# Kernel tuning notes

Hardware: AMD Instinct MI355X
Metric: run time of the kernel (lower is better)

The kernel has to match this reference:

```python
import jax, jax.numpy as jnp
import numpy as np

NH = 1024
VS = 50257
CUT0 = 1675          # round(VS/30)
CUT1 = 3 * CUT0      # 5025
N_CLUSTERS = 2
HEAD_SIZE = CUT0 + N_CLUSTERS          # 1677
D0, D1 = NH // 4, NH // 16             # 256, 64
SZ0, SZ1 = CUT1 - CUT0, VS - CUT1      # 3350, 45232


def setup_inputs() -> dict:
    key = jax.random.key(0)
    ks = jax.random.split(key, 8)
    s = 0.02
    return {
        "x": jax.random.normal(ks[0], (8, 512, NH), dtype=jnp.float32),
        "y": jax.random.randint(ks[1], (8, 512), 0, VS, dtype=jnp.int64),
        "head_w": jax.random.normal(ks[2], (HEAD_SIZE, NH), dtype=jnp.float32) * s,
        "head_b": jnp.zeros((HEAD_SIZE,), dtype=jnp.float32),
        "proj0": jax.random.normal(ks[3], (D0, NH), dtype=jnp.float32) * s,
        "w0": jax.random.normal(ks[4], (SZ0, D0), dtype=jnp.float32) * s,
        "proj1": jax.random.normal(ks[5], (D1, NH), dtype=jnp.float32) * s,
        "w1": jax.random.normal(ks[6], (SZ1, D1), dtype=jnp.float32) * s,
    }


def reference(x, y, head_w, head_b, proj0, w0, proj1, w1):
    # Flatten as in the torch forward: x -> [N, nh], y -> [N]
    xf = x.reshape(-1, x.shape[-1])            # [N, NH]
    yf = y.reshape(-1)                         # [N]

    # Head: shortlist tokens + 2 cluster logits
    head_logits = jnp.einsum('nh,vh->nv', xf, head_w) + head_b   # [N, 1677]
    head_lp = jax.nn.log_softmax(head_logits, axis=-1)

    # Default: target in head shortlist
    in_head = yf < CUT0
    idx_head = jnp.where(in_head, yf, 0)
    out = jnp.take_along_axis(head_lp, idx_head[:, None], axis=1)[:, 0]

    # Tail clusters: dense per-cluster small GEMMs + log-softmax, masked select
    for i, (low, high, proj, w) in enumerate(
            [(CUT0, CUT1, proj0, w0), (CUT1, VS, proj1, w1)]):
        size = high - low
        h = jnp.einsum('nh,dh->nd', xf, proj)          # [N, d_i]
        lp = jax.nn.log_softmax(jnp.einsum('nd,vd->nv', h, w), axis=-1)  # [N, size]
        rel = jnp.clip(yf - low, 0, size - 1)
        cl = head_lp[:, CUT0 + i] + jnp.take_along_axis(lp, rel[:, None], axis=1)[:, 0]
        mask = (yf >= low) & (yf < high)
        out = jnp.where(mask, cl, out)

    loss = -jnp.mean(out)
    return out, loss
```

## Files before the change

### kernel.cpp

```cpp
#include <hip/hip_runtime.h>
#include <stdint.h>

#define NROWS 4096
#define NHID 1024
#define CC0 1675
#define CC1 5025
#define HEADSZ 1677
#define PD0 256
#define PD1 64
#define TSZ0 3350
#define TSZ1 45232
#define HPN (HEADSZ + PD0 + PD1)
#define TPC1 6
#define L2E 1.4426950408889634f
#define LN2 0.6931471805599453f

#define NB_HD 448
#define NB_PJ 96
#define NB_CW 512
#define NB_MID (NB_HD + NB_PJ + NB_CW)

#define NB_C0 864
#define NB_C1 1888
#define NB_TG 1024
#define NB_TAIL (NB_C0 + NB_C1 + NB_TG)

typedef __attribute__((ext_vector_type(8))) __bf16 bf16x8;
typedef __attribute__((ext_vector_type(4))) float f32x4;

__device__ __forceinline__ unsigned short f2bf(float f) {
  union { float f; uint32_t u; } v; v.f = f;
  return (unsigned short)((v.u + 0x7FFFu + ((v.u >> 16) & 1u)) >> 16);
}
__device__ __forceinline__ float bfl(uint32_t u) {
  union { uint32_t u; float f; } v; v.u = u << 16; return v.f;
}
__device__ __forceinline__ float bfh(uint32_t u) {
  union { uint32_t u; float f; } v; v.u = u & 0xFFFF0000u; return v.f;
}
__device__ __forceinline__ float bf1(unsigned short u) {
  union { uint32_t u; float f; } v; v.u = ((uint32_t)u) << 16; return v.f;
}
#define EXP2(x) __builtin_amdgcn_exp2f(x)

#define CV1 1048576
#define CV2 1477888
#define CV3 1543424
#define CV4 1559808
#define CV5 1774208
#define CV6 2497920
#define CVW0 (CV5 - CV4)
#define CVW  (CV6 - CV4)

__global__ void conv_part(const float* __restrict__ x, const float* __restrict__ hw,
                          const float* __restrict__ p0, const float* __restrict__ p1,
                          unsigned short* __restrict__ dst) {
  int stride = gridDim.x * blockDim.x;
  for (int i = blockIdx.x * blockDim.x + threadIdx.x; i < CV4; i += stride) {
    const float* src; int off; float sc;
    if (i < CV1)      { src = x;  off = i;       sc = 1.f; }
    else if (i < CV2) { src = hw; off = i - CV1; sc = L2E; }
    else if (i < CV3) { src = p0; off = i - CV2; sc = 1.f; }
    else              { src = p1; off = i - CV3; sc = 1.f; }
    float4 v = reinterpret_cast<const float4*>(src)[off];
    ushort4 o;
    o.x = f2bf(v.x * sc); o.y = f2bf(v.y * sc);
    o.z = f2bf(v.z * sc); o.w = f2bf(v.w * sc);
    reinterpret_cast<ushort4*>(dst)[i] = o;
  }
}

#define GLOAD(g, l) __builtin_amdgcn_global_load_lds( \
    (const __attribute__((address_space(1))) uint32_t*)(const void*)(g), \
    (__attribute__((address_space(3))) uint32_t*)(void*)(l), 16, 0, 0)

#define SWZB(L) ((L) ^ ((((L) >> 7) & 7) << 4))

__device__ __forceinline__
void gemm_core(const unsigned short* __restrict__ A, int lda,
               const unsigned short* __restrict__ B, int ldb,
               int N, int K, int tile0, int tile1, int brow,
               const float* __restrict__ bias,
               float* __restrict__ sum_out,
               unsigned short* __restrict__ Cout, int ldc, int coutStart,
               unsigned short* AsB, unsigned short* BsB) {
  const int tid = threadIdx.x;
  const int lane = tid & 63;
  const int wid = tid >> 6;
  const int wrow = (wid >> 1) * 64;
  const int wcol = (wid & 1) * 64;
  const int lr = lane & 15, lg = lane >> 4;
  const int nsteps = (tile1 - tile0) * (K >> 5);
  const int rowBase = brow + wrow;

  float sacc[4][4];
#pragma unroll
  for (int m = 0; m < 4; ++m)
#pragma unroll
    for (int r = 0; r < 4; ++r) sacc[m][r] = 0.f;

  auto stage = [&](int b, int tt, int kk) {
#pragma unroll
    for (int c = 0; c < 2; ++c) {
      int g = wid * 128 + c * 64 + lane;
      int L = g * 16;
      int S = SWZB(L);
      int row = S >> 6, ko = (S >> 4) & 3;
      GLOAD(A + (size_t)(brow + row) * lda + kk + ko * 8, (char*)AsB + b * 8192 + L);
      int bsrc = tt * 128 + row; bsrc = bsrc < N ? bsrc : N - 1;
      GLOAD(B + (size_t)bsrc * ldb + kk + ko * 8, (char*)BsB + b * 8192 + L);
    }
  };

  f32x4 acc[4][4];
#pragma unroll
  for (int m = 0; m < 4; ++m)
#pragma unroll
    for (int n = 0; n < 4; ++n) acc[m][n] = (f32x4){0.f, 0.f, 0.f, 0.f};

  int tp = tile0, kp = 0;
  auto adv = [&](int& t, int& k) { k += 32; if (k == K) { k = 0; ++t; } };
  stage(0, tp, kp); adv(tp, kp);
  if (nsteps > 1) { stage(1, tp, kp); adv(tp, kp); }

  int tile = tile0, k0 = 0;
  for (int s = 0; s < nsteps; ++s) {
    if (s + 1 < nsteps) asm volatile("s_waitcnt vmcnt(4)" ::: "memory");
    else                asm volatile("s_waitcnt vmcnt(0)" ::: "memory");
    __builtin_amdgcn_s_barrier();
    if (s + 2 < nsteps) { stage((s + 2) % 3, tp, kp); adv(tp, kp); }

    const int cur = s % 3;
    int k0n = k0 + 32, tn = tile;
    if (k0n == K) { k0n = 0; tn = tile + 1; }

    bf16x8 af[4], bfv[4];
#pragma unroll
    for (int m = 0; m < 4; ++m)
      af[m] = *(const bf16x8*)((const char*)AsB + cur * 8192 +
                               SWZB((wrow + m * 16 + lr) * 64 + lg * 16));
#pragma unroll
    for (int n = 0; n < 4; ++n)
      bfv[n] = *(const bf16x8*)((const char*)BsB + cur * 8192 +
                                SWZB((wcol + n * 16 + lr) * 64 + lg * 16));
#pragma unroll
    for (int m = 0; m < 4; ++m)
#pragma unroll
      for (int n = 0; n < 4; ++n)
        acc[m][n] = __builtin_amdgcn_mfma_f32_16x16x32_bf16(af[m], bfv[n], acc[m][n], 0, 0, 0);

    if (tn != tile) {
      const int cb = tile * 128 + wcol;
#pragma unroll
      for (int m = 0; m < 4; ++m)
#pragma unroll
        for (int n = 0; n < 4; ++n) {
#pragma unroll
          for (int r = 0; r < 4; ++r) {
            int col = cb + n * 16 + lr;
            if (col < N) {
              float v = acc[m][n][r];
              if (Cout && col >= coutStart) {
                int row = rowBase + m * 16 + lg * 4 + r;
                Cout[(size_t)row * ldc + (col - coutStart)] = f2bf(v);
              } else {
                if (bias) v = fmaf(bias[col], L2E, v);
                sacc[m][r] += EXP2(v);
              }
            }
          }
          acc[m][n] = (f32x4){0.f, 0.f, 0.f, 0.f};
        }
    }
    tile = tn; k0 = k0n;
  }

#pragma unroll
  for (int m = 0; m < 4; ++m)
#pragma unroll
    for (int r = 0; r < 4; ++r) {
      float s = sacc[m][r];
      s += __shfl_xor(s, 1); s += __shfl_xor(s, 2);
      s += __shfl_xor(s, 4); s += __shfl_xor(s, 8);
      if (lr == 0) atomicAdd(&sum_out[rowBase + m * 16 + lg * 4 + r], s);
    }
}

__global__ __launch_bounds__(256, 3)
void fused_mid(const unsigned short* __restrict__ xb,
               const unsigned short* __restrict__ hpb,
               const float* __restrict__ head_b,
               float* __restrict__ hs,
               unsigned short* __restrict__ hb,
               float* __restrict__ dm,
               const float* __restrict__ w0f, const float* __restrict__ w1f,
               unsigned short* __restrict__ dstAll) {
  __shared__ __align__(16) unsigned short lds[6 * 4096];
  const int bid = blockIdx.x;

  if (bid < NB_HD) {
    const int xcd = bid & 7;
    const int local = bid >> 3;
    const int rowBlk = xcd * 4 + local / 14;
    const int colChunk = local % 14;
    gemm_core(xb, NHID, hpb, NHID, HEADSZ, NHID, colChunk, colChunk + 1,
              rowBlk * 128, head_b, hs, nullptr, 0, 0, lds, lds + 3 * 4096);
    return;
  }

  if (bid < NB_HD + NB_PJ) {
    const int b1 = bid - NB_HD;
    const int cpx = NB_PJ >> 3;
    const int sid = (b1 & 7) * cpx + (b1 >> 3);
    const int rowBlk = sid & 31;
    const int colChunk = sid >> 5;
    gemm_core(xb, NHID, hpb + (size_t)HEADSZ * NHID, NHID, PD0 + PD1, NHID,
              colChunk, colChunk + 1, rowBlk * 128,
              nullptr, dm, hb, PD0 + PD1, 0, lds, lds + 3 * 4096);
    return;
  }

  {
    const int b2 = bid - NB_HD - NB_PJ;
    const int stride = NB_CW * 256;
    for (int i = b2 * 256 + (int)threadIdx.x; i < CVW; i += stride) {
      const float* src; int off;
      if (i < CVW0) { src = w0f; off = i; }
      else          { src = w1f; off = i - CVW0; }
      float4 v = reinterpret_cast<const float4*>(src)[off];
      ushort4 o;
      o.x = f2bf(v.x * L2E); o.y = f2bf(v.y * L2E);
      o.z = f2bf(v.z * L2E); o.w = f2bf(v.w * L2E);
      reinterpret_cast<ushort4*>(dstAll)[CV4 + i] = o;
    }
  }
}

__global__ __launch_bounds__(256, 3)
void fused_tail(const unsigned short* __restrict__ hb,
                const unsigned short* __restrict__ w0b,
                const unsigned short* __restrict__ w1b,
                const unsigned short* __restrict__ xb,
                const unsigned short* __restrict__ hwb,
                const float* __restrict__ head_b,
                const int* __restrict__ y,
                float* __restrict__ s0, float* __restrict__ s1,
                float* __restrict__ ht, float* __restrict__ tc) {
  __shared__ __align__(16) unsigned short lds[6 * 4096];
  const int bid = blockIdx.x;

  if (bid < NB_C0) {
    const int cpx = NB_C0 >> 3;
    const int sid = (bid & 7) * cpx + (bid >> 3);
    const int rowBlk = sid & 31;
    const int colChunk = sid >> 5;
    gemm_core(hb, PD0 + PD1, w0b, PD0, TSZ0, PD0, colChunk, colChunk + 1,
              rowBlk * 128, nullptr, s0, nullptr, 0, 0, lds, lds + 3 * 4096);
    return;
  }

  if (bid < NB_C0 + NB_C1) {
    const int b1 = bid - NB_C0;
    const int tid = threadIdx.x;
    const int lane = tid & 63;
    const int wid = tid >> 6;
    const int lr = lane & 15, lg = lane >> 4;
    const int cpx = NB_C1 >> 3;
    const int sid = (b1 & 7) * cpx + (b1 >> 3);
    const int rowBlk = sid & 31;
    const int colChunk = sid >> 5;
    const int rowBase = rowBlk * 128 + (wid >> 1) * 64;
    const int wcol = (wid & 1) * 64;
    const int tile0 = colChunk * TPC1;

    int colOff[4], srcOff[4];
#pragma unroll
    for (int c = 0; c < 4; ++c) {
      int L = (c * 256 + tid) * 16;
      int S = L ^ (((L >> 7) & 7) << 4);
      colOff[c] = S >> 7;
      srcOff[c] = (S & 127) >> 1;
    }
    auto stage = [&](int b, int t) {
#pragma unroll
      for (int c = 0; c < 4; ++c) {
        int gc = t * 128 + colOff[c];
        gc = gc < TSZ1 ? gc : TSZ1 - 1;
        GLOAD(w1b + (size_t)gc * PD1 + srcOff[c],
              (char*)lds + b * 16384 + (c * 256 + tid) * 16);
      }
    };

    bf16x8 af[4][2];
#pragma unroll
    for (int m = 0; m < 4; ++m) {
      const unsigned short* p = hb + PD0 +
          (size_t)(rowBase + m * 16 + lr) * (PD0 + PD1) + lg * 8;
      af[m][0] = *(const bf16x8*)p;
      af[m][1] = *(const bf16x8*)(p + 32);
    }

    float sacc[4][4];
#pragma unroll
    for (int m = 0; m < 4; ++m)
#pragma unroll
      for (int r = 0; r < 4; ++r) sacc[m][r] = 0.f;

    stage(0, tile0);
    stage(1, tile0 + 1);

#pragma unroll 1
    for (int s = 0; s < TPC1; ++s) {
      if (s + 1 < TPC1) asm volatile("s_waitcnt vmcnt(4)" ::: "memory");
      else              asm volatile("s_waitcnt vmcnt(0)" ::: "memory");
      __builtin_amdgcn_s_barrier();
      if (s + 2 < TPC1) stage((s + 2) % 3, tile0 + s + 2);

      const int cur = s % 3;
      const int cb = (tile0 + s) * 128 + wcol;
      const int full = (cb + 63 < TSZ1);

#pragma unroll
      for (int nh = 0; nh < 2; ++nh) {
        bf16x8 bf[2][2];
#pragma unroll
        for (int nn = 0; nn < 2; ++nn) {
          int ccol = wcol + (nh * 2 + nn) * 16 + lr;
#pragma unroll
          for (int kh = 0; kh < 2; ++kh) {
            int L = ccol * 128 + kh * 64 + lg * 16;
            bf[nn][kh] = *(const bf16x8*)((const char*)lds + cur * 16384 +
                                          (L ^ ((ccol & 7) << 4)));
          }
        }
        f32x4 acc[4][2];
#pragma unroll
        for (int m = 0; m < 4; ++m)
#pragma unroll
          for (int nn = 0; nn < 2; ++nn) {
            f32x4 a = (f32x4){0.f, 0.f, 0.f, 0.f};
            a = __builtin_amdgcn_mfma_f32_16x16x32_bf16(af[m][0], bf[nn][0], a, 0, 0, 0);
            a = __builtin_amdgcn_mfma_f32_16x16x32_bf16(af[m][1], bf[nn][1], a, 0, 0, 0);
            acc[m][nn] = a;
          }
        if (full) {
#pragma unroll
          for (int m = 0; m < 4; ++m)
#pragma unroll
            for (int r = 0; r < 4; ++r)
              sacc[m][r] += EXP2(acc[m][0][r]) + EXP2(acc[m][1][r]);
        } else {
#pragma unroll
          for (int m = 0; m < 4; ++m)
#pragma unroll
            for (int r = 0; r < 4; ++r) {
              float t = 0.f;
#pragma unroll
              for (int nn = 0; nn < 2; ++nn)
                if (cb + (nh * 2 + nn) * 16 + lr < TSZ1) t += EXP2(acc[m][nn][r]);
              sacc[m][r] += t;
            }
        }
      }
    }

#pragma unroll
    for (int m = 0; m < 4; ++m)
#pragma unroll
      for (int r = 0; r < 4; ++r) {
        float s = sacc[m][r];
        s += __shfl_xor(s, 1); s += __shfl_xor(s, 2);
        s += __shfl_xor(s, 4); s += __shfl_xor(s, 8);
        if (lr == 0) atomicAdd(&s1[rowBase + m * 16 + lg * 4 + r], s);
      }
    return;
  }

  {
    const int b2 = bid - NB_C0 - NB_C1;
    int row = b2 * 4 + (threadIdx.x >> 6);
    int lane = threadIdx.x & 63;
    int yv = y[row];
    int th = yv < CC0 ? yv : (yv < CC1 ? CC0 : CC0 + 1);

    const unsigned short* xr = xb + (size_t)row * NHID + lane * 16;
    const unsigned short* wr = hwb + (size_t)th * NHID + lane * 16;
    uint4 xa = *(const uint4*)xr,       wa = *(const uint4*)wr;
    uint4 xc = *(const uint4*)(xr + 8), wc = *(const uint4*)(wr + 8);
    float s = 0.f;
    uint32_t xs[8] = {xa.x, xa.y, xa.z, xa.w, xc.x, xc.y, xc.z, xc.w};
    uint32_t ws[8] = {wa.x, wa.y, wa.z, wa.w, wc.x, wc.y, wc.z, wc.w};
#pragma unroll
    for (int j = 0; j < 8; ++j)
      s += bfl(xs[j]) * bfl(ws[j]) + bfh(xs[j]) * bfh(ws[j]);
#pragma unroll
    for (int d = 1; d < 64; d <<= 1) s += __shfl_xor(s, d);

    float cl = 0.f;
    if (yv >= CC0) {
      if (yv < CC1) {
        int rel = yv - CC0;
        const unsigned short* hr = hb + (size_t)row * (PD0 + PD1) + lane * 4;
        const unsigned short* w0r = w0b + (size_t)rel * PD0 + lane * 4;
        uint2 ha = *(const uint2*)hr, wa0 = *(const uint2*)w0r;
        cl = bfl(ha.x) * bfl(wa0.x) + bfh(ha.x) * bfh(wa0.x)
           + bfl(ha.y) * bfl(wa0.y) + bfh(ha.y) * bfh(wa0.y);
      } else {
        int rel = yv - CC1;
        cl = bf1(hb[(size_t)row * (PD0 + PD1) + PD0 + lane])
           * bf1(w1b[(size_t)rel * PD1 + lane]);
      }
#pragma unroll
      for (int d = 1; d < 64; d <<= 1) cl += __shfl_xor(cl, d);
    }
    if (lane == 0) { ht[row] = s * LN2 + head_b[th]; tc[row] = (yv < CC0) ? 0.f : cl; }
  }
}

__global__ void rowloss(const float* __restrict__ hs, const float* __restrict__ ht,
                        const float* __restrict__ s0, const float* __restrict__ s1,
                        const float* __restrict__ tc,
                        const int* __restrict__ y, float* __restrict__ out) {
  int n = blockIdx.x * 256 + threadIdx.x;
  int yv = y[n];
  float o = ht[n] - __builtin_amdgcn_logf(hs[n]) * LN2;
  if (yv >= CC0)
    o += tc[n] * LN2 - __builtin_amdgcn_logf(yv < CC1 ? s0[n] : s1[n]) * LN2;
  out[n] = o;
  float l = o;
#pragma unroll
  for (int d = 1; d < 64; d <<= 1) l += __shfl_xor(l, d);
  __shared__ float red[4];
  if ((threadIdx.x & 63) == 0) red[threadIdx.x >> 6] = l;
  __syncthreads();
  if (threadIdx.x == 0)
    atomicAdd(&out[NROWS], -(red[0] + red[1] + red[2] + red[3]) / (float)NROWS);
}

extern "C" void kernel_launch(void* const* d_in, const int* in_sizes, int n_in,
                              void* d_out, int out_size, void* d_ws, size_t ws_size,
                              hipStream_t stream) {
  const float* x      = (const float*)d_in[0];
  const int*   y      = (const int*)d_in[1];
  const float* head_w = (const float*)d_in[2];
  const float* head_b = (const float*)d_in[3];
  const float* proj0  = (const float*)d_in[4];
  const float* w0     = (const float*)d_in[5];
  const float* proj1  = (const float*)d_in[6];
  const float* w1     = (const float*)d_in[7];
  float* out = (float*)d_out;

  char* wp = (char*)d_ws;
  unsigned short* xb  = (unsigned short*)wp; wp += (size_t)NROWS * NHID * 2;
  unsigned short* hpb = (unsigned short*)wp; wp += (size_t)HPN * NHID * 2;
  unsigned short* w0b = (unsigned short*)wp; wp += (size_t)TSZ0 * PD0 * 2;
  unsigned short* w1b = (unsigned short*)wp; wp += (size_t)TSZ1 * PD1 * 2;
  unsigned short* hb  = (unsigned short*)wp; wp += (size_t)NROWS * (PD0 + PD1) * 2;
  float* hs = (float*)wp; wp += NROWS * 4;
  float* s0 = (float*)wp; wp += NROWS * 4;
  float* s1 = (float*)wp; wp += NROWS * 4;
  float* ht = (float*)wp; wp += NROWS * 4;
  float* tc = (float*)wp; wp += NROWS * 4;
  float* dm = (float*)wp; wp += NROWS * 4;

  hipMemsetAsync(hs, 0, 3 * NROWS * 4, stream);
  hipMemsetAsync(out + NROWS, 0, 4, stream);

  conv_part<<<dim3(1024), 256, 0, stream>>>(x, head_w, proj0, proj1, xb);

  fused_mid<<<dim3(NB_MID), 256, 0, stream>>>(
      xb, hpb, head_b, hs, hb, dm, w0, w1, xb);

  fused_tail<<<dim3(NB_TAIL), 256, 0, stream>>>(
      hb, w0b, w1b, xb, hpb, head_b, y, s0, s1, ht, tc);

  rowloss<<<dim3(NROWS / 256), 256, 0, stream>>>(hs, ht, s0, s1, tc, y, out);
}
```

Measured before the change: 104.9 us.

## Run tail kernel with 512-thread blocks and 8 waves per tile

The tail kernel now launches 512-thread blocks. Each 128x128 output tile is split across 8 waves, each owning 64 rows by 32 columns, instead of 4 waves owning 64 by 64. A new gemm_core512 variant handles the cluster-0 GEMM under the new layout, and the target-gather section now covers 8 rows per block with half as many blocks. The aim is more waves in flight and fewer accumulator registers per wave to hide latency, at the cost of more redundant A-fragment loads and barrier participants per tile.

```diff
diff --git a/kernel.cpp b/kernel.cpp
--- a/kernel.cpp
+++ b/kernel.cpp
@@ -22,7 +22,7 @@
 
 #define NB_C0 864
 #define NB_C1 1888
-#define NB_TG 1024
+#define NB_TG 512
 #define NB_TAIL (NB_C0 + NB_C1 + NB_TG)
 
 typedef __attribute__((ext_vector_type(8))) __bf16 bf16x8;
@@ -186,6 +186,92 @@
     }
 }
 
+__device__ __forceinline__
+void gemm_core512(const unsigned short* __restrict__ A, int lda,
+                  const unsigned short* __restrict__ B, int ldb,
+                  int N, int K, int tile0, int brow,
+                  float* __restrict__ sum_out,
+                  unsigned short* AsB, unsigned short* BsB) {
+  const int tid = threadIdx.x;
+  const int lane = tid & 63;
+  const int wid = tid >> 6;
+  const int wrow = (wid >> 2) * 64;
+  const int wcol = (wid & 3) * 32;
+  const int lr = lane & 15, lg = lane >> 4;
+  const int nsteps = K >> 5;
+  const int rowBase = brow + wrow;
+
+  float sacc[4][4];
+#pragma unroll
+  for (int m = 0; m < 4; ++m)
+#pragma unroll
+    for (int r = 0; r < 4; ++r) sacc[m][r] = 0.f;
+
+  const int L0 = tid * 16;
+  const int S0 = SWZB(L0);
+  const int arow = S0 >> 6, ako = ((S0 >> 4) & 3) * 8;
+
+  auto stage = [&](int b, int kk) {
+    GLOAD(A + (size_t)(brow + arow) * lda + kk + ako, (char*)AsB + b * 8192 + L0);
+    int bsrc = tile0 * 128 + arow; bsrc = bsrc < N ? bsrc : N - 1;
+    GLOAD(B + (size_t)bsrc * ldb + kk + ako, (char*)BsB + b * 8192 + L0);
+  };
+
+  f32x4 acc[4][2];
+#pragma unroll
+  for (int m = 0; m < 4; ++m)
+#pragma unroll
+    for (int n = 0; n < 2; ++n) acc[m][n] = (f32x4){0.f, 0.f, 0.f, 0.f};
+
+  stage(0, 0);
+  if (nsteps > 1) stage(1, 32);
+
+  for (int s = 0; s < nsteps; ++s) {
+    if (s + 1 < nsteps) asm volatile("s_waitcnt vmcnt(2)" ::: "memory");
+    else                asm volatile("s_waitcnt vmcnt(0)" ::: "memory");
+    __builtin_amdgcn_s_barrier();
+    if (s + 2 < nsteps) stage((s + 2) % 3, (s + 2) * 32);
+
+    const int cur = s % 3;
+    bf16x8 af[4], bfv[2];
+#pragma unroll
+    for (int m = 0; m < 4; ++m)
+      af[m] = *(const bf16x8*)((const char*)AsB + cur * 8192 +
+                               SWZB((wrow + m * 16 + lr) * 64 + lg * 16));
+#pragma unroll
+    for (int n = 0; n < 2; ++n)
+      bfv[n] = *(const bf16x8*)((const char*)BsB + cur * 8192 +
+                                SWZB((wcol + n * 16 + lr) * 64 + lg * 16));
+#pragma unroll
+    for (int m = 0; m < 4; ++m)
+#pragma unroll
+      for (int n = 0; n < 2; ++n)
+        acc[m][n] = __builtin_amdgcn_mfma_f32_16x16x32_bf16(af[m], bfv[n], acc[m][n], 0, 0, 0);
+  }
+
+  const int cb = tile0 * 128 + wcol;
+#pragma unroll
+  for (int m = 0; m < 4; ++m)
+#pragma unroll
+    for (int n = 0; n < 2; ++n) {
+      int col = cb + n * 16 + lr;
+      if (col < N) {
+#pragma unroll
+        for (int r = 0; r < 4; ++r) sacc[m][r] += EXP2(acc[m][n][r]);
+      }
+    }
+
+#pragma unroll
+  for (int m = 0; m < 4; ++m)
+#pragma unroll
+    for (int r = 0; r < 4; ++r) {
+      float s = sacc[m][r];
+      s += __shfl_xor(s, 1); s += __shfl_xor(s, 2);
+      s += __shfl_xor(s, 4); s += __shfl_xor(s, 8);
+      if (lr == 0) atomicAdd(&sum_out[rowBase + m * 16 + lg * 4 + r], s);
+    }
+}
+
 __global__ __launch_bounds__(256, 3)
 void fused_mid(const unsigned short* __restrict__ xb,
                const unsigned short* __restrict__ hpb,
@@ -236,7 +322,7 @@
   }
 }
 
-__global__ __launch_bounds__(256, 3)
+__global__ __launch_bounds__(512, 4)
 void fused_tail(const unsigned short* __restrict__ hb,
                 const unsigned short* __restrict__ w0b,
                 const unsigned short* __restrict__ w1b,
@@ -254,8 +340,8 @@
     const int sid = (bid & 7) * cpx + (bid >> 3);
     const int rowBlk = sid & 31;
     const int colChunk = sid >> 5;
-    gemm_core(hb, PD0 + PD1, w0b, PD0, TSZ0, PD0, colChunk, colChunk + 1,
-              rowBlk * 128, nullptr, s0, nullptr, 0, 0, lds, lds + 3 * 4096);
+    gemm_core512(hb, PD0 + PD1, w0b, PD0, TSZ0, PD0, colChunk,
+                 rowBlk * 128, s0, lds, lds + 3 * 4096);
     return;
   }
 
@@ -269,25 +355,25 @@
     const int sid = (b1 & 7) * cpx + (b1 >> 3);
     const int rowBlk = sid & 31;
     const int colChunk = sid >> 5;
-    const int rowBase = rowBlk * 128 + (wid >> 1) * 64;
-    const int wcol = (wid & 1) * 64;
+    const int rowBase = rowBlk * 128 + (wid >> 2) * 64;
+    const int wcol = (wid & 3) * 32;
     const int tile0 = colChunk * TPC1;
 
-    int colOff[4], srcOff[4];
-#pragma unroll
-    for (int c = 0; c < 4; ++c) {
-      int L = (c * 256 + tid) * 16;
+    int colOff[2], srcOff[2];
+#pragma unroll
+    for (int c = 0; c < 2; ++c) {
+      int L = (c * 512 + tid) * 16;
       int S = L ^ (((L >> 7) & 7) << 4);
       colOff[c] = S >> 7;
       srcOff[c] = (S & 127) >> 1;
     }
     auto stage = [&](int b, int t) {
 #pragma unroll
-      for (int c = 0; c < 4; ++c) {
+      for (int c = 0; c < 2; ++c) {
         int gc = t * 128 + colOff[c];
         gc = gc < TSZ1 ? gc : TSZ1 - 1;
         GLOAD(w1b + (size_t)gc * PD1 + srcOff[c],
-              (char*)lds + b * 16384 + (c * 256 + tid) * 16);
+              (char*)lds + b * 16384 + (c * 512 + tid) * 16);
       }
     };
 
@@ -311,56 +397,53 @@
 
 #pragma unroll 1
     for (int s = 0; s < TPC1; ++s) {
-      if (s + 1 < TPC1) asm volatile("s_waitcnt vmcnt(4)" ::: "memory");
+      if (s + 1 < TPC1) asm volatile("s_waitcnt vmcnt(2)" ::: "memory");
       else              asm volatile("s_waitcnt vmcnt(0)" ::: "memory");
       __builtin_amdgcn_s_barrier();
       if (s + 2 < TPC1) stage((s + 2) % 3, tile0 + s + 2);
 
       const int cur = s % 3;
       const int cb = (tile0 + s) * 128 + wcol;
-      const int full = (cb + 63 < TSZ1);
-
-#pragma unroll
-      for (int nh = 0; nh < 2; ++nh) {
-        bf16x8 bf[2][2];
+      const int full = (cb + 31 < TSZ1);
+
+      bf16x8 bf[2][2];
+#pragma unroll
+      for (int nn = 0; nn < 2; ++nn) {
+        int ccol = wcol + nn * 16 + lr;
+#pragma unroll
+        for (int kh = 0; kh < 2; ++kh) {
+          int L = ccol * 128 + kh * 64 + lg * 16;
+          bf[nn][kh] = *(const bf16x8*)((const char*)lds + cur * 16384 +
+                                        (L ^ ((ccol & 7) << 4)));
+        }
+      }
+      f32x4 acc[4][2];
+#pragma unroll
+      for (int m = 0; m < 4; ++m)
 #pragma unroll
         for (int nn = 0; nn < 2; ++nn) {
-          int ccol = wcol + (nh * 2 + nn) * 16 + lr;
-#pragma unroll
-          for (int kh = 0; kh < 2; ++kh) {
-            int L = ccol * 128 + kh * 64 + lg * 16;
-            bf[nn][kh] = *(const bf16x8*)((const char*)lds + cur * 16384 +
-                                          (L ^ ((ccol & 7) << 4)));
+          f32x4 a = (f32x4){0.f, 0.f, 0.f, 0.f};
+          a = __builtin_amdgcn_mfma_f32_16x16x32_bf16(af[m][0], bf[nn][0], a, 0, 0, 0);
+          a = __builtin_amdgcn_mfma_f32_16x16x32_bf16(af[m][1], bf[nn][1], a, 0, 0, 0);
+          acc[m][nn] = a;
+        }
+      if (full) {
+#pragma unroll
+        for (int m = 0; m < 4; ++m)
+#pragma unroll
+          for (int r = 0; r < 4; ++r)
+            sacc[m][r] += EXP2(acc[m][0][r]) + EXP2(acc[m][1][r]);
+      } else {
+#pragma unroll
+        for (int m = 0; m < 4; ++m)
+#pragma unroll
+          for (int r = 0; r < 4; ++r) {
+            float t = 0.f;
+#pragma unroll
+            for (int nn = 0; nn < 2; ++nn)
+              if (cb + nn * 16 + lr < TSZ1) t += EXP2(acc[m][nn][r]);
+            sacc[m][r] += t;
           }
-        }
-        f32x4 acc[4][2];
-#pragma unroll
-        for (int m = 0; m < 4; ++m)
-#pragma unroll
-          for (int nn = 0; nn < 2; ++nn) {
-            f32x4 a = (f32x4){0.f, 0.f, 0.f, 0.f};
-            a = __builtin_amdgcn_mfma_f32_16x16x32_bf16(af[m][0], bf[nn][0], a, 0, 0, 0);
-            a = __builtin_amdgcn_mfma_f32_16x16x32_bf16(af[m][1], bf[nn][1], a, 0, 0, 0);
-            acc[m][nn] = a;
-          }
-        if (full) {
-#pragma unroll
-          for (int m = 0; m < 4; ++m)
-#pragma unroll
-            for (int r = 0; r < 4; ++r)
-              sacc[m][r] += EXP2(acc[m][0][r]) + EXP2(acc[m][1][r]);
-        } else {
-#pragma unroll
-          for (int m = 0; m < 4; ++m)
-#pragma unroll
-            for (int r = 0; r < 4; ++r) {
-              float t = 0.f;
-#pragma unroll
-              for (int nn = 0; nn < 2; ++nn)
-                if (cb + (nh * 2 + nn) * 16 + lr < TSZ1) t += EXP2(acc[m][nn][r]);
-              sacc[m][r] += t;
-            }
-        }
       }
     }
 
@@ -378,7 +461,7 @@
 
   {
     const int b2 = bid - NB_C0 - NB_C1;
-    int row = b2 * 4 + (threadIdx.x >> 6);
+    int row = b2 * 8 + (threadIdx.x >> 6);
     int lane = threadIdx.x & 63;
     int yv = y[row];
     int th = yv < CC0 ? yv : (yv < CC1 ? CC0 : CC0 + 1);
@@ -471,7 +554,7 @@
   fused_mid<<<dim3(NB_MID), 256, 0, stream>>>(
       xb, hpb, head_b, hs, hb, dm, w0, w1, xb);
 
-  fused_tail<<<dim3(NB_TAIL), 256, 0, stream>>>(
+  fused_tail<<<dim3(NB_TAIL), 512, 0, stream>>>(
       hb, w0b, w1b, xb, hpb, head_b, y, s0, s1, ht, tc);
 
   rowloss<<<dim3(NROWS / 256), 256, 0, stream>>>(hs, ht, s0, s1, tc, y, out);
```

Result: slower. 119.4 us (+13.8%).

## Give each wave a private LDS slice in cluster-1 tail GEMM, drop block barriers

Applied to the files above, without the earlier changes.

Reworks the cluster-1 tail sum-of-exp GEMM so each wave stages its own 32-column slice of w1 into a private LDS region, so the per-tile block-wide barrier is no longer needed. Row blocks shrink to 64 rows and column chunks grow to 12 tiles, with a bounded tail chunk, giving 1920 blocks. The cluster-1 blocks now come first in the grid, ahead of the cluster-0 and target blocks. The aim is to cut barrier stalls and let the large tail work start early, at the cost of less cross-wave reuse of staged w1 data and more reloads of the h operand per column.

```diff
diff --git a/kernel.cpp b/kernel.cpp
--- a/kernel.cpp
+++ b/kernel.cpp
@@ -11,7 +11,8 @@
 #define TSZ0 3350
 #define TSZ1 45232
 #define HPN (HEADSZ + PD0 + PD1)
-#define TPC1 6
+#define NT1 354
+#define TPC1 12
 #define L2E 1.4426950408889634f
 #define LN2 0.6931471805599453f
 
@@ -20,10 +21,10 @@
 #define NB_CW 512
 #define NB_MID (NB_HD + NB_PJ + NB_CW)
 
+#define NB_C1 1920
 #define NB_C0 864
-#define NB_C1 1888
 #define NB_TG 1024
-#define NB_TAIL (NB_C0 + NB_C1 + NB_TG)
+#define NB_TAIL (NB_C1 + NB_C0 + NB_TG)
 
 typedef __attribute__((ext_vector_type(8))) __bf16 bf16x8;
 typedef __attribute__((ext_vector_type(4))) float f32x4;
@@ -249,34 +250,27 @@
   __shared__ __align__(16) unsigned short lds[6 * 4096];
   const int bid = blockIdx.x;
 
-  if (bid < NB_C0) {
-    const int cpx = NB_C0 >> 3;
-    const int sid = (bid & 7) * cpx + (bid >> 3);
-    const int rowBlk = sid & 31;
-    const int colChunk = sid >> 5;
-    gemm_core(hb, PD0 + PD1, w0b, PD0, TSZ0, PD0, colChunk, colChunk + 1,
-              rowBlk * 128, nullptr, s0, nullptr, 0, 0, lds, lds + 3 * 4096);
-    return;
-  }
-
-  if (bid < NB_C0 + NB_C1) {
-    const int b1 = bid - NB_C0;
+  if (bid < NB_C1) {
     const int tid = threadIdx.x;
     const int lane = tid & 63;
     const int wid = tid >> 6;
     const int lr = lane & 15, lg = lane >> 4;
     const int cpx = NB_C1 >> 3;
-    const int sid = (b1 & 7) * cpx + (b1 >> 3);
-    const int rowBlk = sid & 31;
-    const int colChunk = sid >> 5;
-    const int rowBase = rowBlk * 128 + (wid >> 1) * 64;
-    const int wcol = (wid & 1) * 64;
+    const int sid = (bid & 7) * cpx + (bid >> 3);
+    const int rowBlk = sid & 63;
+    const int colChunk = sid >> 6;
+    const int rowBase = rowBlk * 64;
+    const int wcol = wid * 32;
     const int tile0 = colChunk * TPC1;
+    const int tile1 = min(tile0 + TPC1, NT1);
+    const int nt = tile1 - tile0;
+
+    char* slice = (char*)lds + wid * 12288;
 
     int colOff[4], srcOff[4];
 #pragma unroll
     for (int c = 0; c < 4; ++c) {
-      int L = (c * 256 + tid) * 16;
+      int L = c * 1024 + lane * 16;
       int S = L ^ (((L >> 7) & 7) << 4);
       colOff[c] = S >> 7;
       srcOff[c] = (S & 127) >> 1;
@@ -284,10 +278,10 @@
     auto stage = [&](int b, int t) {
 #pragma unroll
       for (int c = 0; c < 4; ++c) {
-        int gc = t * 128 + colOff[c];
+        int gc = t * 128 + wcol + colOff[c];
         gc = gc < TSZ1 ? gc : TSZ1 - 1;
         GLOAD(w1b + (size_t)gc * PD1 + srcOff[c],
-              (char*)lds + b * 16384 + (c * 256 + tid) * 16);
+              slice + b * 4096 + c * 1024 + lane * 16);
       }
     };
 
@@ -307,60 +301,58 @@
       for (int r = 0; r < 4; ++r) sacc[m][r] = 0.f;
 
     stage(0, tile0);
-    stage(1, tile0 + 1);
+    if (nt > 1) stage(1, tile0 + 1);
 
 #pragma unroll 1
-    for (int s = 0; s < TPC1; ++s) {
-      if (s + 1 < TPC1) asm volatile("s_waitcnt vmcnt(4)" ::: "memory");
-      else              asm volatile("s_waitcnt vmcnt(0)" ::: "memory");
-      __builtin_amdgcn_s_barrier();
-      if (s + 2 < TPC1) stage((s + 2) % 3, tile0 + s + 2);
-
+    for (int s = 0; s < nt; ++s) {
+      if (s + 1 < nt) asm volatile("s_waitcnt vmcnt(4)" ::: "memory");
+      else            asm volatile("s_waitcnt vmcnt(0)" ::: "memory");
       const int cur = s % 3;
+
+      bf16x8 bf[2][2];
+#pragma unroll
+      for (int nn = 0; nn < 2; ++nn) {
+        int lc = nn * 16 + lr;
+#pragma unroll
+        for (int kh = 0; kh < 2; ++kh) {
+          int L = lc * 128 + kh * 64 + lg * 16;
+          bf[nn][kh] = *(const bf16x8*)(slice + cur * 4096 +
+                                        (L ^ ((lc & 7) << 4)));
+        }
+      }
+      asm volatile("s_waitcnt lgkmcnt(0)" ::: "memory");
+      __builtin_amdgcn_sched_barrier(0);
+      if (s + 2 < nt) stage((s + 2) % 3, tile0 + s + 2);
+
+      f32x4 acc[4][2];
+#pragma unroll
+      for (int m = 0; m < 4; ++m)
+#pragma unroll
+        for (int nn = 0; nn < 2; ++nn) {
+          f32x4 a = (f32x4){0.f, 0.f, 0.f, 0.f};
+          a = __builtin_amdgcn_mfma_f32_16x16x32_bf16(af[m][0], bf[nn][0], a, 0, 0, 0);
+          a = __builtin_amdgcn_mfma_f32_16x16x32_bf16(af[m][1], bf[nn][1], a, 0, 0, 0);
+          acc[m][nn] = a;
+        }
+
       const int cb = (tile0 + s) * 128 + wcol;
-      const int full = (cb + 63 < TSZ1);
-
-#pragma unroll
-      for (int nh = 0; nh < 2; ++nh) {
-        bf16x8 bf[2][2];
-#pragma unroll
-        for (int nn = 0; nn < 2; ++nn) {
-          int ccol = wcol + (nh * 2 + nn) * 16 + lr;
-#pragma unroll
-          for (int kh = 0; kh < 2; ++kh) {
-            int L = ccol * 128 + kh * 64 + lg * 16;
-            bf[nn][kh] = *(const bf16x8*)((const char*)lds + cur * 16384 +
-                                          (L ^ ((ccol & 7) << 4)));
+      if (cb + 31 < TSZ1) {
+#pragma unroll
+        for (int m = 0; m < 4; ++m)
+#pragma unroll
+          for (int r = 0; r < 4; ++r)
+            sacc[m][r] += EXP2(acc[m][0][r]) + EXP2(acc[m][1][r]);
+      } else {
+#pragma unroll
+        for (int m = 0; m < 4; ++m)
+#pragma unroll
+          for (int r = 0; r < 4; ++r) {
+            float t = 0.f;
+#pragma unroll
+            for (int nn = 0; nn < 2; ++nn)
+              if (cb + nn * 16 + lr < TSZ1) t += EXP2(acc[m][nn][r]);
+            sacc[m][r] += t;
           }
-        }
-        f32x4 acc[4][2];
-#pragma unroll
-        for (int m = 0; m < 4; ++m)
-#pragma unroll
-          for (int nn = 0; nn < 2; ++nn) {
-            f32x4 a = (f32x4){0.f, 0.f, 0.f, 0.f};
-            a = __builtin_amdgcn_mfma_f32_16x16x32_bf16(af[m][0], bf[nn][0], a, 0, 0, 0);
-            a = __builtin_amdgcn_mfma_f32_16x16x32_bf16(af[m][1], bf[nn][1], a, 0, 0, 0);
-            acc[m][nn] = a;
-          }
-        if (full) {
-#pragma unroll
-          for (int m = 0; m < 4; ++m)
-#pragma unroll
-            for (int r = 0; r < 4; ++r)
-              sacc[m][r] += EXP2(acc[m][0][r]) + EXP2(acc[m][1][r]);
-        } else {
-#pragma unroll
-          for (int m = 0; m < 4; ++m)
-#pragma unroll
-            for (int r = 0; r < 4; ++r) {
-              float t = 0.f;
-#pragma unroll
-              for (int nn = 0; nn < 2; ++nn)
-                if (cb + (nh * 2 + nn) * 16 + lr < TSZ1) t += EXP2(acc[m][nn][r]);
-              sacc[m][r] += t;
-            }
-        }
       }
     }
 
@@ -376,8 +368,19 @@
     return;
   }
 
+  if (bid < NB_C1 + NB_C0) {
+    const int b0 = bid - NB_C1;
+    const int cpx = NB_C0 >> 3;
+    const int sid = (b0 & 7) * cpx + (b0 >> 3);
+    const int rowBlk = sid & 31;
+    const int colChunk = sid >> 5;
+    gemm_core(hb, PD0 + PD1, w0b, PD0, TSZ0, PD0, colChunk, colChunk + 1,
+              rowBlk * 128, nullptr, s0, nullptr, 0, 0, lds, lds + 3 * 4096);
+    return;
+  }
+
   {
-    const int b2 = bid - NB_C0 - NB_C1;
+    const int b2 = bid - NB_C1 - NB_C0;
     int row = b2 * 4 + (threadIdx.x >> 6);
     int lane = threadIdx.x & 63;
     int yv = y[row];
```

Result: slower. 110.8 us (+5.7%).

## Compact tail-cluster rows by target and skip GEMM blocks for absent rows

Applied to the files above, without the earlier changes.

An extra block in the conversion kernel prefix-sums row indices whose target falls in each tail cluster and builds gather and position maps. The tail cluster GEMMs read A rows through these index lists and return early for row blocks beyond the cluster's row count, so each cluster's softmax normaliser is computed only for rows that need it. The row-loss kernel reads sums through the position maps. This adds a serial single-thread scan and indirect loads, and the saving depends on the label distribution, which is uniform here, so most rows fall in cluster 1.

```diff
diff --git a/kernel.cpp b/kernel.cpp
--- a/kernel.cpp
+++ b/kernel.cpp
@@ -20,10 +20,10 @@
 #define NB_CW 512
 #define NB_MID (NB_HD + NB_PJ + NB_CW)
 
+#define NB_C1 1888
 #define NB_C0 864
-#define NB_C1 1888
 #define NB_TG 1024
-#define NB_TAIL (NB_C0 + NB_C1 + NB_TG)
+#define NB_TAIL (NB_C1 + NB_C0 + NB_TG)
 
 typedef __attribute__((ext_vector_type(8))) __bf16 bf16x8;
 typedef __attribute__((ext_vector_type(4))) float f32x4;
@@ -54,9 +54,47 @@
 
 __global__ void conv_part(const float* __restrict__ x, const float* __restrict__ hw,
                           const float* __restrict__ p0, const float* __restrict__ p1,
-                          unsigned short* __restrict__ dst) {
-  int stride = gridDim.x * blockDim.x;
-  for (int i = blockIdx.x * blockDim.x + threadIdx.x; i < CV4; i += stride) {
+                          unsigned short* __restrict__ dst,
+                          const int* __restrict__ y,
+                          int* __restrict__ idx0, int* __restrict__ pos0,
+                          int* __restrict__ idx1, int* __restrict__ pos1,
+                          int* __restrict__ n01) {
+  if (blockIdx.x == 1024) {
+    __shared__ int sc0[256], sc1[256], nsh[2];
+    int t = threadIdx.x;
+    int yl[16];
+    int c0 = 0, c1 = 0;
+#pragma unroll
+    for (int k = 0; k < 16; ++k) {
+      int yv = y[t * 16 + k];
+      yl[k] = yv;
+      c0 += (yv >= CC0 && yv < CC1);
+      c1 += (yv >= CC1);
+    }
+    sc0[t] = c0; sc1[t] = c1;
+    __syncthreads();
+    if (t == 0) {
+      int a0 = 0, a1 = 0;
+      for (int i = 0; i < 256; ++i) {
+        int v0 = sc0[i]; sc0[i] = a0; a0 += v0;
+        int v1 = sc1[i]; sc1[i] = a1; a1 += v1;
+      }
+      n01[0] = a0; n01[1] = a1; nsh[0] = a0; nsh[1] = a1;
+    }
+    __syncthreads();
+    int p0c = sc0[t], p1c = sc1[t];
+#pragma unroll
+    for (int k = 0; k < 16; ++k) {
+      int n = t * 16 + k, yv = yl[k];
+      if (yv >= CC0 && yv < CC1) { idx0[p0c] = n; pos0[n] = p0c; ++p0c; }
+      else if (yv >= CC1)        { idx1[p1c] = n; pos1[n] = p1c; ++p1c; }
+    }
+    for (int j = nsh[0] + t; j < NROWS; j += 256) idx0[j] = 0;
+    for (int j = nsh[1] + t; j < NROWS; j += 256) idx1[j] = 0;
+    return;
+  }
+  const int stride = 1024 * 256;
+  for (int i = blockIdx.x * 256 + threadIdx.x; i < CV4; i += stride) {
     const float* src; int off; float sc;
     if (i < CV1)      { src = x;  off = i;       sc = 1.f; }
     else if (i < CV2) { src = hw; off = i - CV1; sc = L2E; }
@@ -83,7 +121,8 @@
                const float* __restrict__ bias,
                float* __restrict__ sum_out,
                unsigned short* __restrict__ Cout, int ldc, int coutStart,
-               unsigned short* AsB, unsigned short* BsB) {
+               unsigned short* AsB, unsigned short* BsB,
+               const int* __restrict__ gidx) {
   const int tid = threadIdx.x;
   const int lane = tid & 63;
   const int wid = tid >> 6;
@@ -93,6 +132,15 @@
   const int nsteps = (tile1 - tile0) * (K >> 5);
   const int rowBase = brow + wrow;
 
+  int arowc[2];
+#pragma unroll
+  for (int c = 0; c < 2; ++c) {
+    int g = wid * 128 + c * 64 + lane;
+    int S = SWZB(g * 16);
+    int row = S >> 6;
+    arowc[c] = gidx ? gidx[brow + row] : brow + row;
+  }
+
   float sacc[4][4];
 #pragma unroll
   for (int m = 0; m < 4; ++m)
@@ -106,7 +154,7 @@
       int L = g * 16;
       int S = SWZB(L);
       int row = S >> 6, ko = (S >> 4) & 3;
-      GLOAD(A + (size_t)(brow + row) * lda + kk + ko * 8, (char*)AsB + b * 8192 + L);
+      GLOAD(A + (size_t)arowc[c] * lda + kk + ko * 8, (char*)AsB + b * 8192 + L);
       int bsrc = tt * 128 + row; bsrc = bsrc < N ? bsrc : N - 1;
       GLOAD(B + (size_t)bsrc * ldb + kk + ko * 8, (char*)BsB + b * 8192 + L);
     }
@@ -204,7 +252,8 @@
     const int rowBlk = xcd * 4 + local / 14;
     const int colChunk = local % 14;
     gemm_core(xb, NHID, hpb, NHID, HEADSZ, NHID, colChunk, colChunk + 1,
-              rowBlk * 128, head_b, hs, nullptr, 0, 0, lds, lds + 3 * 4096);
+              rowBlk * 128, head_b, hs, nullptr, 0, 0,
+              lds, lds + 3 * 4096, nullptr);
     return;
   }
 
@@ -216,7 +265,7 @@
     const int colChunk = sid >> 5;
     gemm_core(xb, NHID, hpb + (size_t)HEADSZ * NHID, NHID, PD0 + PD1, NHID,
               colChunk, colChunk + 1, rowBlk * 128,
-              nullptr, dm, hb, PD0 + PD1, 0, lds, lds + 3 * 4096);
+              nullptr, dm, hb, PD0 + PD1, 0, lds, lds + 3 * 4096, nullptr);
     return;
   }
 
@@ -244,31 +293,23 @@
                 const unsigned short* __restrict__ hwb,
                 const float* __restrict__ head_b,
                 const int* __restrict__ y,
+                const int* __restrict__ idx0, const int* __restrict__ idx1,
+                const int* __restrict__ n01,
                 float* __restrict__ s0, float* __restrict__ s1,
                 float* __restrict__ ht, float* __restrict__ tc) {
   __shared__ __align__(16) unsigned short lds[6 * 4096];
   const int bid = blockIdx.x;
 
-  if (bid < NB_C0) {
-    const int cpx = NB_C0 >> 3;
-    const int sid = (bid & 7) * cpx + (bid >> 3);
-    const int rowBlk = sid & 31;
-    const int colChunk = sid >> 5;
-    gemm_core(hb, PD0 + PD1, w0b, PD0, TSZ0, PD0, colChunk, colChunk + 1,
-              rowBlk * 128, nullptr, s0, nullptr, 0, 0, lds, lds + 3 * 4096);
-    return;
-  }
-
-  if (bid < NB_C0 + NB_C1) {
-    const int b1 = bid - NB_C0;
+  if (bid < NB_C1) {
     const int tid = threadIdx.x;
     const int lane = tid & 63;
     const int wid = tid >> 6;
     const int lr = lane & 15, lg = lane >> 4;
     const int cpx = NB_C1 >> 3;
-    const int sid = (b1 & 7) * cpx + (b1 >> 3);
+    const int sid = (bid & 7) * cpx + (bid >> 3);
     const int rowBlk = sid & 31;
     const int colChunk = sid >> 5;
+    if (rowBlk * 128 >= n01[1]) return;
     const int rowBase = rowBlk * 128 + (wid >> 1) * 64;
     const int wcol = (wid & 1) * 64;
     const int tile0 = colChunk * TPC1;
@@ -294,8 +335,9 @@
     bf16x8 af[4][2];
 #pragma unroll
     for (int m = 0; m < 4; ++m) {
+      int ridx = idx1[rowBase + m * 16 + lr];
       const unsigned short* p = hb + PD0 +
-          (size_t)(rowBase + m * 16 + lr) * (PD0 + PD1) + lg * 8;
+          (size_t)ridx * (PD0 + PD1) + lg * 8;
       af[m][0] = *(const bf16x8*)p;
       af[m][1] = *(const bf16x8*)(p + 32);
     }
@@ -376,8 +418,21 @@
     return;
   }
 
+  if (bid < NB_C1 + NB_C0) {
+    const int b0 = bid - NB_C1;
+    const int cpx = NB_C0 >> 3;
+    const int sid = (b0 & 7) * cpx + (b0 >> 3);
+    const int rowBlk = sid & 31;
+    const int colChunk = sid >> 5;
+    if (rowBlk * 128 >= n01[0]) return;
+    gemm_core(hb, PD0 + PD1, w0b, PD0, TSZ0, PD0, colChunk, colChunk + 1,
+              rowBlk * 128, nullptr, s0, nullptr, 0, 0,
+              lds, lds + 3 * 4096, idx0);
+    return;
+  }
+
   {
-    const int b2 = bid - NB_C0 - NB_C1;
+    const int b2 = bid - NB_C1 - NB_C0;
     int row = b2 * 4 + (threadIdx.x >> 6);
     int lane = threadIdx.x & 63;
     int yv = y[row];
@@ -420,12 +475,15 @@
 __global__ void rowloss(const float* __restrict__ hs, const float* __restrict__ ht,
                         const float* __restrict__ s0, const float* __restrict__ s1,
                         const float* __restrict__ tc,
+                        const int* __restrict__ pos0, const int* __restrict__ pos1,
                         const int* __restrict__ y, float* __restrict__ out) {
   int n = blockIdx.x * 256 + threadIdx.x;
   int yv = y[n];
   float o = ht[n] - __builtin_amdgcn_logf(hs[n]) * LN2;
-  if (yv >= CC0)
-    o += tc[n] * LN2 - __builtin_amdgcn_logf(yv < CC1 ? s0[n] : s1[n]) * LN2;
+  if (yv >= CC0) {
+    float sv = (yv < CC1) ? s0[pos0[n]] : s1[pos1[n]];
+    o += tc[n] * LN2 - __builtin_amdgcn_logf(sv) * LN2;
+  }
   out[n] = o;
   float l = o;
 #pragma unroll
@@ -462,17 +520,24 @@
   float* ht = (float*)wp; wp += NROWS * 4;
   float* tc = (float*)wp; wp += NROWS * 4;
   float* dm = (float*)wp; wp += NROWS * 4;
+  int* idx0 = (int*)wp; wp += NROWS * 4;
+  int* pos0 = (int*)wp; wp += NROWS * 4;
+  int* idx1 = (int*)wp; wp += NROWS * 4;
+  int* pos1 = (int*)wp; wp += NROWS * 4;
+  int* n01  = (int*)wp; wp += 8 * 4;
 
   hipMemsetAsync(hs, 0, 3 * NROWS * 4, stream);
   hipMemsetAsync(out + NROWS, 0, 4, stream);
 
-  conv_part<<<dim3(1024), 256, 0, stream>>>(x, head_w, proj0, proj1, xb);
+  conv_part<<<dim3(1025), 256, 0, stream>>>(
+      x, head_w, proj0, proj1, xb, y, idx0, pos0, idx1, pos1, n01);
 
   fused_mid<<<dim3(NB_MID), 256, 0, stream>>>(
       xb, hpb, head_b, hs, hb, dm, w0, w1, xb);
 
   fused_tail<<<dim3(NB_TAIL), 256, 0, stream>>>(
-      hb, w0b, w1b, xb, hpb, head_b, y, s0, s1, ht, tc);
-
-  rowloss<<<dim3(NROWS / 256), 256, 0, stream>>>(hs, ht, s0, s1, tc, y, out);
-}
+      hb, w0b, w1b, xb, hpb, head_b, y, idx0, idx1, n01, s0, s1, ht, tc);
+
+  rowloss<<<dim3(NROWS / 256), 256, 0, stream>>>(
+      hs, ht, s0, s1, tc, pos0, pos1, y, out);
+}
```

Result: no change. 105.0 us (+0.1%).
